# Optimization experiments

Hardware: AMD Instinct MI355X
Metric: run time of the kernel (lower is better)

Reference implementation:

```python
import jax, jax.numpy as jnp
import numpy as np

N = 100000   # nodes
E = 1200000  # edges
D = 64       # feature dim (in_channels == out_channels)


def gcn_layer(x, W, src, dst):
    # GCNConv(normalize=False, bias=False, aggr='add'):
    # linear transform then scatter-add of source messages into targets.
    h = x @ W                                            # [N, D]
    msg = h[src]                                         # [E, D] gather
    return jax.ops.segment_sum(msg, dst, num_segments=x.shape[0])  # [N, D]


def setup_inputs() -> dict:
    key = jax.random.key(0)
    ks = jax.random.split(key, 5)
    x = jax.random.normal(ks[0], (N, D), dtype=jnp.float32)
    edge_index = jax.random.randint(ks[1], (2, E), 0, N, dtype=jnp.int64)
    scale = 1.0 / np.sqrt(D).astype(np.float32)
    W0 = jax.random.normal(ks[2], (D, D), dtype=jnp.float32) * scale
    W1 = jax.random.normal(ks[3], (D, D), dtype=jnp.float32) * scale
    W2 = jax.random.normal(ks[4], (D, D), dtype=jnp.float32) * scale
    return {"x": x, "edge_index": edge_index, "W0": W0, "W1": W1, "W2": W2}


def reference(x, edge_index, W0, W1, W2):
    src = edge_index[0]  # messages flow source -> target (PyG default)
    dst = edge_index[1]
    # num_hop = 3 stacked convs; dropout p=0 and use_bn=False are no-ops.
    for W in (W0, W1, W2):
        x = gcn_layer(x, W, src, dst)
    return x
```

## Files before the change

kernel.cpp:

```cpp
#include <hip/hip_runtime.h>


#define GCN_D 64
#define SEGSHIFT 8
#define SEGROWS 256
#define MAXSEG 512
#define A_EPB 4096

typedef unsigned short ushort;

__device__ __forceinline__ float bf2f(ushort u) {
    union { unsigned u; float f; } c; c.u = ((unsigned)u) << 16; return c.f;
}
__device__ __forceinline__ ushort f2bf(float f) {
    union { float f; unsigned u; } c; c.f = f;
    const unsigned r = 0x7FFFu + ((c.u >> 16) & 1u);
    return (ushort)((c.u + r) >> 16);
}

__global__ __launch_bounds__(256) void k_wchain(const float* __restrict__ W0,
                                                const float* __restrict__ W1,
                                                const float* __restrict__ W2,
                                                float* __restrict__ Wc) {
    __shared__ float A[4096], B[4096], T[4096];
    const int t = threadIdx.x;
    for (int i = t; i < 1024; i += 256) {
        ((float4*)A)[i] = ((const float4*)W0)[i];
        ((float4*)B)[i] = ((const float4*)W1)[i];
    }
    __syncthreads();
#pragma unroll
    for (int g = 0; g < 4; ++g) {
        const int idx = t + 256 * g;
        const int r = idx >> 4, c4 = idx & 15;
        float4 acc = make_float4(0.f, 0.f, 0.f, 0.f);
#pragma unroll
        for (int k = 0; k < 64; ++k) {
            const float a = A[r * 64 + k];
            const float4 b = ((float4*)B)[k * 16 + c4];
            acc.x = fmaf(a, b.x, acc.x); acc.y = fmaf(a, b.y, acc.y);
            acc.z = fmaf(a, b.z, acc.z); acc.w = fmaf(a, b.w, acc.w);
        }
        ((float4*)T)[idx] = acc;
    }
    __syncthreads();
    for (int i = t; i < 1024; i += 256) ((float4*)B)[i] = ((const float4*)W2)[i];
    __syncthreads();
#pragma unroll
    for (int g = 0; g < 4; ++g) {
        const int idx = t + 256 * g;
        const int r = idx >> 4, c4 = idx & 15;
        float4 acc = make_float4(0.f, 0.f, 0.f, 0.f);
#pragma unroll
        for (int k = 0; k < 64; ++k) {
            const float a = T[r * 64 + k];
            const float4 b = ((float4*)B)[k * 16 + c4];
            acc.x = fmaf(a, b.x, acc.x); acc.y = fmaf(a, b.y, acc.y);
            acc.z = fmaf(a, b.z, acc.z); acc.w = fmaf(a, b.w, acc.w);
        }
        ((float4*)Wc)[idx] = acc;
    }
}

__global__ __launch_bounds__(256) void k_tobf(const float* __restrict__ X,
                                              ushort* __restrict__ B,
                                              int* __restrict__ ghist, long long n4) {
    if (blockIdx.x == 0) {
        for (int i = threadIdx.x; i < MAXSEG; i += 256) ghist[i] = 0;
    }
    const long long stride = (long long)gridDim.x * 256;
    for (long long i = blockIdx.x * 256ll + threadIdx.x; i < n4; i += stride) {
        const float4 v = ((const float4*)X)[i];
        ushort4 u;
        u.x = f2bf(v.x); u.y = f2bf(v.y); u.z = f2bf(v.z); u.w = f2bf(v.w);
        ((ushort4*)B)[i] = u;
    }
}

__global__ __launch_bounds__(256) void k_a0(const int* __restrict__ ei,
                                            int* __restrict__ ghist, int E) {
    __shared__ int h[MAXSEG];
    const int t = threadIdx.x;
    for (int i = t; i < MAXSEG; i += 256) h[i] = 0;
    __syncthreads();
    for (int e = blockIdx.x * 256 + t; e < E; e += gridDim.x * 256)
        atomicAdd(&h[ei[E + e] >> SEGSHIFT], 1);
    __syncthreads();
    for (int i = t; i < MAXSEG; i += 256) {
        const int c = h[i];
        if (c) atomicAdd(&ghist[i], c);
    }
}

__global__ __launch_bounds__(MAXSEG) void k_ascan(const int* __restrict__ ghist,
                                                  int* __restrict__ gOff,
                                                  int* __restrict__ gcur,
                                                  int* __restrict__ rp, int N, int E) {
    __shared__ int sd[MAXSEG];
    const int t = threadIdx.x;
    const int v = ghist[t];
    sd[t] = v; __syncthreads();
    for (int off = 1; off < MAXSEG; off <<= 1) {
        const int y = (t >= off) ? sd[t - off] : 0;
        __syncthreads();
        sd[t] += y;
        __syncthreads();
    }
    const int excl = sd[t] - v;
    gOff[t] = excl; gcur[t] = excl;
    if (t == MAXSEG - 1) gOff[MAXSEG] = sd[t];
    if (t == 0) rp[N] = E;
}

__global__ __launch_bounds__(512) void k_apart(const int* __restrict__ ei,
                                               int* __restrict__ gcur,
                                               unsigned* __restrict__ ebuf, int E) {
    __shared__ int hist[MAXSEG], lofs[MAXSEG], cur[MAXSEG], gbase[MAXSEG];
    __shared__ unsigned stg[A_EPB];
    const int t = threadIdx.x;
    const int base = blockIdx.x * A_EPB;
    const int cnt = min(A_EPB, E - base);

    hist[t] = 0;
    __syncthreads();

    unsigned my[8]; int mb[8];
#pragma unroll
    for (int j = 0; j < 8; ++j) {
        const int i = t + j * 512;
        if (i < cnt) {
            const int e = base + i;
            const unsigned s = (unsigned)ei[e];
            const unsigned d = (unsigned)ei[E + e];
            my[j] = (s << 8) | (d & (SEGROWS - 1));
            mb[j] = (int)(d >> SEGSHIFT);
            atomicAdd(&hist[mb[j]], 1);
        } else mb[j] = -1;
    }
    __syncthreads();

    {
        const int v = hist[t];
        lofs[t] = v; __syncthreads();
        for (int off = 1; off < MAXSEG; off <<= 1) {
            const int y = (t >= off) ? lofs[t - off] : 0;
            __syncthreads();
            lofs[t] += y;
            __syncthreads();
        }
        const int excl = lofs[t] - v;
        __syncthreads();
        lofs[t] = excl; cur[t] = excl;
    }
    __syncthreads();

#pragma unroll
    for (int j = 0; j < 8; ++j) {
        if (mb[j] >= 0) {
            const int p = atomicAdd(&cur[mb[j]], 1);
            stg[p] = my[j];
        }
    }
    __syncthreads();

    {
        const int c = hist[t];
        gbase[t] = c ? atomicAdd(&gcur[t], c) : 0;
    }
    __syncthreads();

    for (int i = t; i < cnt; i += 512) {
        int lo = 0, hi = MAXSEG - 1;
        while (lo < hi) {
            const int mid = (lo + hi + 1) >> 1;
            if (lofs[mid] <= i) lo = mid; else hi = mid - 1;
        }
        ebuf[(size_t)gbase[lo] + (unsigned)(i - lofs[lo])] = stg[i];
    }
}

__global__ __launch_bounds__(SEGROWS) void k_bplace(const unsigned* __restrict__ ebuf,
                                                    const int* __restrict__ gOff,
                                                    int* __restrict__ rp,
                                                    int* __restrict__ cs, int N) {
    __shared__ int h[SEGROWS], ofs[SEGROWS];
    const int s = blockIdx.x;
    const int t = threadIdx.x;
    const int e0 = gOff[s];
    const int e1 = gOff[s + 1];

    h[t] = 0; __syncthreads();
    for (int e = e0 + t; e < e1; e += SEGROWS)
        atomicAdd(&h[ebuf[e] & (SEGROWS - 1)], 1);
    __syncthreads();

    const int v = h[t];
    ofs[t] = v; __syncthreads();
    for (int off = 1; off < SEGROWS; off <<= 1) {
        const int y = (t >= off) ? ofs[t - off] : 0;
        __syncthreads();
        ofs[t] += y;
        __syncthreads();
    }
    const int excl = ofs[t] - v;
    const int r = s * SEGROWS + t;
    if (r < N) rp[r] = e0 + excl;
    __syncthreads();
    ofs[t] = excl;
    __syncthreads();

    for (int e = e0 + t; e < e1; e += SEGROWS) {
        const unsigned pr = ebuf[e];
        const int lr = (int)(pr & (SEGROWS - 1));
        const int p = atomicAdd(&ofs[lr], 1);
        cs[e0 + p] = (int)(pr >> 8);
    }
}

__global__ __launch_bounds__(256) void k_aggc(const ushort* __restrict__ B,
                                              const int* __restrict__ rp,
                                              const int* __restrict__ cs,
                                              ushort* __restrict__ out, int N) {
    const int t = threadIdx.x;
    const int gw = (blockIdx.x * 256 + t) >> 6;
    const int lane = t & 63;
    const int f4 = lane & 15;
    const int r = gw * 4 + (lane >> 4);
    if (r >= N) return;

    const int e0 = rp[r];
    const int e1 = rp[r + 1];
    const ushort4* Bv = (const ushort4*)B;

    float4 acc = make_float4(0.f, 0.f, 0.f, 0.f);
    int e = e0;
    for (; e + 7 < e1; e += 8) {
        ushort4 u[8];
#pragma unroll
        for (int j = 0; j < 8; ++j) u[j] = Bv[(size_t)cs[e + j] * 16 + f4];
#pragma unroll
        for (int j = 0; j < 8; ++j) {
            acc.x += bf2f(u[j].x); acc.y += bf2f(u[j].y);
            acc.z += bf2f(u[j].z); acc.w += bf2f(u[j].w);
        }
    }
    for (; e + 3 < e1; e += 4) {
        ushort4 u[4];
#pragma unroll
        for (int j = 0; j < 4; ++j) u[j] = Bv[(size_t)cs[e + j] * 16 + f4];
#pragma unroll
        for (int j = 0; j < 4; ++j) {
            acc.x += bf2f(u[j].x); acc.y += bf2f(u[j].y);
            acc.z += bf2f(u[j].z); acc.w += bf2f(u[j].w);
        }
    }
    for (; e < e1; ++e) {
        const ushort4 u = Bv[(size_t)cs[e] * 16 + f4];
        acc.x += bf2f(u.x); acc.y += bf2f(u.y);
        acc.z += bf2f(u.z); acc.w += bf2f(u.w);
    }
    ushort4 o;
    o.x = f2bf(acc.x); o.y = f2bf(acc.y); o.z = f2bf(acc.z); o.w = f2bf(acc.w);
    ((ushort4*)out)[(size_t)r * 16 + f4] = o;
}

__global__ __launch_bounds__(256) void k_aggf(const ushort* __restrict__ B,
                                              const int* __restrict__ rp,
                                              const int* __restrict__ cs,
                                              const float* __restrict__ Wc,
                                              float* __restrict__ out, int N) {
    __shared__ float Wl[64 * 64];
    __shared__ float Xl[16][65];
    const int t = threadIdx.x;
    for (int i = t; i < 1024; i += 256) ((float4*)Wl)[i] = ((const float4*)Wc)[i];

    const int lr = t >> 4;
    const int f4 = t & 15;
    const int r = blockIdx.x * 16 + lr;

    float4 acc = make_float4(0.f, 0.f, 0.f, 0.f);
    if (r < N) {
        const int e0 = rp[r];
        const int e1 = rp[r + 1];
        const ushort4* Bv = (const ushort4*)B;
        int e = e0;
        for (; e + 7 < e1; e += 8) {
            ushort4 u[8];
#pragma unroll
            for (int j = 0; j < 8; ++j) u[j] = Bv[(size_t)cs[e + j] * 16 + f4];
#pragma unroll
            for (int j = 0; j < 8; ++j) {
                acc.x += bf2f(u[j].x); acc.y += bf2f(u[j].y);
                acc.z += bf2f(u[j].z); acc.w += bf2f(u[j].w);
            }
        }
        for (; e + 3 < e1; e += 4) {
            ushort4 u[4];
#pragma unroll
            for (int j = 0; j < 4; ++j) u[j] = Bv[(size_t)cs[e + j] * 16 + f4];
#pragma unroll
            for (int j = 0; j < 4; ++j) {
                acc.x += bf2f(u[j].x); acc.y += bf2f(u[j].y);
                acc.z += bf2f(u[j].z); acc.w += bf2f(u[j].w);
            }
        }
        for (; e < e1; ++e) {
            const ushort4 u = Bv[(size_t)cs[e] * 16 + f4];
            acc.x += bf2f(u.x); acc.y += bf2f(u.y);
            acc.z += bf2f(u.z); acc.w += bf2f(u.w);
        }
    }
    Xl[lr][f4 * 4 + 0] = bf2f(f2bf(acc.x));
    Xl[lr][f4 * 4 + 1] = bf2f(f2bf(acc.y));
    Xl[lr][f4 * 4 + 2] = bf2f(f2bf(acc.z));
    Xl[lr][f4 * 4 + 3] = bf2f(f2bf(acc.w));
    __syncthreads();

    float4 g = make_float4(0.f, 0.f, 0.f, 0.f);
#pragma unroll
    for (int k = 0; k < 64; ++k) {
        const float xv = Xl[lr][k];
        const float4 w4 = ((const float4*)Wl)[k * 16 + f4];
        g.x = fmaf(xv, w4.x, g.x); g.y = fmaf(xv, w4.y, g.y);
        g.z = fmaf(xv, w4.z, g.z); g.w = fmaf(xv, w4.w, g.w);
    }
    if (r < N) ((float4*)out)[(size_t)r * 16 + f4] = g;
}

__global__ __launch_bounds__(256) void gcn_gemm64(const float* __restrict__ X,
                                                  const float* __restrict__ W,
                                                  float* __restrict__ H,
                                                  int nrows) {
    __shared__ float Wl[64 * 64];
    __shared__ float Xl[16][65];
    const int tid = threadIdx.x;
    for (int i = tid; i < 1024; i += 256) ((float4*)Wl)[i] = ((const float4*)W)[i];
    const int rowBase = blockIdx.x * 16;
    const int lr = tid >> 4;
    const int lc = tid & 15;
    const int grow = rowBase + lr;
    if (grow < nrows) {
        float4 xv = ((const float4*)X)[(long long)grow * 16 + lc];
        Xl[lr][lc * 4 + 0] = xv.x; Xl[lr][lc * 4 + 1] = xv.y;
        Xl[lr][lc * 4 + 2] = xv.z; Xl[lr][lc * 4 + 3] = xv.w;
    }
    __syncthreads();
    float4 acc = make_float4(0.f, 0.f, 0.f, 0.f);
#pragma unroll
    for (int k = 0; k < 64; ++k) {
        const float xv = Xl[lr][k];
        const float4 w4 = ((float4*)Wl)[k * 16 + lc];
        acc.x = fmaf(xv, w4.x, acc.x); acc.y = fmaf(xv, w4.y, acc.y);
        acc.z = fmaf(xv, w4.z, acc.z); acc.w = fmaf(xv, w4.w, acc.w);
    }
    if (grow < nrows) ((float4*)H)[(long long)grow * 16 + lc] = acc;
}

__global__ __launch_bounds__(256) void gcn_scatter(const float* __restrict__ H,
                                                   const int* __restrict__ ei,
                                                   float* __restrict__ out,
                                                   int nedges) {
    const long long t = (long long)blockIdx.x * 256 + threadIdx.x;
    const int e = (int)(t >> 4);
    if (e >= nedges) return;
    const int lc = (int)(t & 15);
    const int s = ei[e];
    const int d = ei[nedges + e];
    const float4 v = ((const float4*)H)[(long long)s * 16 + lc];
    float* o = out + (long long)d * GCN_D + lc * 4;
    atomicAdd(o + 0, v.x);
    atomicAdd(o + 1, v.y);
    atomicAdd(o + 2, v.z);
    atomicAdd(o + 3, v.w);
}

extern "C" void kernel_launch(void* const* d_in, const int* in_sizes, int n_in,
                              void* d_out, int out_size, void* d_ws, size_t ws_size,
                              hipStream_t stream) {
    const float* x  = (const float*)d_in[0];
    const int*   ei = (const int*)d_in[1];
    const float* W0 = (const float*)d_in[2];
    const float* W1 = (const float*)d_in[3];
    const float* W2 = (const float*)d_in[4];
    float* out = (float*)d_out;

    const int N_ = in_sizes[0] / GCN_D;
    const int E_ = in_sizes[1] / 2;
    const int NSEG = (N_ + SEGROWS - 1) >> SEGSHIFT;

    uintptr_t base = (uintptr_t)d_ws;
    ushort* B0 = (ushort*)base;
    const size_t bfBytes  = (size_t)N_ * GCN_D * 2;
    const size_t regBytes = bfBytes > (size_t)E_ * 4 ? bfBytes : (size_t)E_ * 4;
    ushort*   B1   = (ushort*)(base + bfBytes);
    unsigned* ebuf = (unsigned*)B1;
    int* rp    = (int*)(base + bfBytes + regBytes);
    int* gOff  = rp + (N_ + 2);
    int* ghist = gOff + (MAXSEG + 1);
    int* gcur  = ghist + MAXSEG;
    float* Wc  = (float*)(gcur + MAXSEG);
    int* cs    = (int*)(Wc + 4096);
    const size_t needed = ((uintptr_t)(cs + E_) - base);

    const int gemmBlocks = (N_ + 15) / 16;

    if (NSEG <= MAXSEG && N_ < (1 << 24) && ws_size >= needed) {
        k_wchain<<<1, 256, 0, stream>>>(W0, W1, W2, Wc);
        k_tobf<<<1024, 256, 0, stream>>>(x, B0, ghist, (long long)N_ * 16);
        k_a0<<<512, 256, 0, stream>>>(ei, ghist, E_);
        k_ascan<<<1, MAXSEG, 0, stream>>>(ghist, gOff, gcur, rp, N_, E_);
        k_apart<<<(E_ + A_EPB - 1) / A_EPB, 512, 0, stream>>>(ei, gcur, ebuf, E_);
        k_bplace<<<NSEG, SEGROWS, 0, stream>>>(ebuf, gOff, rp, cs, N_);

        const int aggBlocks = (N_ + 15) / 16;
        k_aggc<<<aggBlocks, 256, 0, stream>>>(B0, rp, cs, B1, N_);
        k_aggc<<<aggBlocks, 256, 0, stream>>>(B1, rp, cs, B0, N_);
        k_aggf<<<aggBlocks, 256, 0, stream>>>(B0, rp, cs, Wc, out, N_);
    } else {
        float* h = (float*)d_ws;
        const int scatBlocks = (int)(((long long)E_ * 16 + 255) / 256);
        const float* curAct = x;
        for (int l = 0; l < 3; ++l) {
            const float* Wl = (l == 0) ? W0 : (l == 1) ? W1 : W2;
            gcn_gemm64<<<gemmBlocks, 256, 0, stream>>>(curAct, Wl, h, N_);
            hipMemsetAsync(out, 0, (size_t)N_ * GCN_D * sizeof(float), stream);
            gcn_scatter<<<scatBlocks, 256, 0, stream>>>(h, ei, out, E_);
            curAct = out;
        }
    }
}
```

Baseline: 177.1 us.

## Apply combined weight before aggregation and drop binary search in partition

The product of the three weight matrices is now applied to x up front in a GEMM that writes bf16, replacing the plain bf16 conversion. This leaves the last aggregation as a pure gather-sum with no shared-memory GEMM or block barrier. It relies on the layers being linear, and it changes where bf16 rounding happens relative to the reference. Separately, the partition kernel stores each edge's bucket id in shared memory, replacing a per-element binary search over bucket offsets, and the histogram zeroing moves into the weight-chain kernel.

Measured after the change: 172.4 us. -2.7%, faster.

```diff
diff --git a/kernel.cpp b/kernel.cpp
--- a/kernel.cpp
+++ b/kernel.cpp
@@ -21,9 +21,11 @@
 __global__ __launch_bounds__(256) void k_wchain(const float* __restrict__ W0,
                                                 const float* __restrict__ W1,
                                                 const float* __restrict__ W2,
-                                                float* __restrict__ Wc) {
+                                                float* __restrict__ Wc,
+                                                int* __restrict__ ghist) {
     __shared__ float A[4096], B[4096], T[4096];
     const int t = threadIdx.x;
+    for (int i = t; i < MAXSEG; i += 256) ghist[i] = 0;
     for (int i = t; i < 1024; i += 256) {
         ((float4*)A)[i] = ((const float4*)W0)[i];
         ((float4*)B)[i] = ((const float4*)W1)[i];
@@ -62,18 +64,38 @@
     }
 }
 
-__global__ __launch_bounds__(256) void k_tobf(const float* __restrict__ X,
-                                              ushort* __restrict__ B,
-                                              int* __restrict__ ghist, long long n4) {
-    if (blockIdx.x == 0) {
-        for (int i = threadIdx.x; i < MAXSEG; i += 256) ghist[i] = 0;
-    }
-    const long long stride = (long long)gridDim.x * 256;
-    for (long long i = blockIdx.x * 256ll + threadIdx.x; i < n4; i += stride) {
-        const float4 v = ((const float4*)X)[i];
-        ushort4 u;
-        u.x = f2bf(v.x); u.y = f2bf(v.y); u.z = f2bf(v.z); u.w = f2bf(v.w);
-        ((ushort4*)B)[i] = u;
+__global__ __launch_bounds__(256) void k_gemmcvt(const float* __restrict__ X,
+                                                 const float* __restrict__ Wc,
+                                                 ushort* __restrict__ B,
+                                                 int nrows) {
+    __shared__ float Wl[64 * 64];
+    __shared__ float Xl[16][65];
+    const int tid = threadIdx.x;
+    for (int i = tid; i < 1024; i += 256) ((float4*)Wl)[i] = ((const float4*)Wc)[i];
+
+    const int lr = tid >> 4;
+    const int lc = tid & 15;
+    const int grow = blockIdx.x * 16 + lr;
+
+    if (grow < nrows) {
+        const float4 xv = ((const float4*)X)[(size_t)grow * 16 + lc];
+        Xl[lr][lc * 4 + 0] = xv.x; Xl[lr][lc * 4 + 1] = xv.y;
+        Xl[lr][lc * 4 + 2] = xv.z; Xl[lr][lc * 4 + 3] = xv.w;
+    }
+    __syncthreads();
+
+    float4 acc = make_float4(0.f, 0.f, 0.f, 0.f);
+#pragma unroll
+    for (int k = 0; k < 64; ++k) {
+        const float xv = Xl[lr][k];
+        const float4 w4 = ((const float4*)Wl)[k * 16 + lc];
+        acc.x = fmaf(xv, w4.x, acc.x); acc.y = fmaf(xv, w4.y, acc.y);
+        acc.z = fmaf(xv, w4.z, acc.z); acc.w = fmaf(xv, w4.w, acc.w);
+    }
+    if (grow < nrows) {
+        ushort4 o;
+        o.x = f2bf(acc.x); o.y = f2bf(acc.y); o.z = f2bf(acc.z); o.w = f2bf(acc.w);
+        ((ushort4*)B)[(size_t)grow * 16 + lc] = o;
     }
 }
 
@@ -117,6 +139,7 @@
                                                unsigned* __restrict__ ebuf, int E) {
     __shared__ int hist[MAXSEG], lofs[MAXSEG], cur[MAXSEG], gbase[MAXSEG];
     __shared__ unsigned stg[A_EPB];
+    __shared__ ushort stg2[A_EPB];
     const int t = threadIdx.x;
     const int base = blockIdx.x * A_EPB;
     const int cnt = min(A_EPB, E - base);
@@ -159,6 +182,7 @@
         if (mb[j] >= 0) {
             const int p = atomicAdd(&cur[mb[j]], 1);
             stg[p] = my[j];
+            stg2[p] = (ushort)mb[j];
         }
     }
     __syncthreads();
@@ -170,12 +194,8 @@
     __syncthreads();
 
     for (int i = t; i < cnt; i += 512) {
-        int lo = 0, hi = MAXSEG - 1;
-        while (lo < hi) {
-            const int mid = (lo + hi + 1) >> 1;
-            if (lofs[mid] <= i) lo = mid; else hi = mid - 1;
-        }
-        ebuf[(size_t)gbase[lo] + (unsigned)(i - lofs[lo])] = stg[i];
+        const int b = (int)stg2[i];
+        ebuf[(size_t)gbase[b] + (unsigned)(i - lofs[b])] = stg[i];
     }
 }
 
@@ -264,67 +284,49 @@
     ((ushort4*)out)[(size_t)r * 16 + f4] = o;
 }
 
-__global__ __launch_bounds__(256) void k_aggf(const ushort* __restrict__ B,
+__global__ __launch_bounds__(256) void k_aggw(const ushort* __restrict__ B,
                                               const int* __restrict__ rp,
                                               const int* __restrict__ cs,
-                                              const float* __restrict__ Wc,
                                               float* __restrict__ out, int N) {
-    __shared__ float Wl[64 * 64];
-    __shared__ float Xl[16][65];
-    const int t = threadIdx.x;
-    for (int i = t; i < 1024; i += 256) ((float4*)Wl)[i] = ((const float4*)Wc)[i];
-
-    const int lr = t >> 4;
-    const int f4 = t & 15;
-    const int r = blockIdx.x * 16 + lr;
+    const int t = threadIdx.x;
+    const int gw = (blockIdx.x * 256 + t) >> 6;
+    const int lane = t & 63;
+    const int f4 = lane & 15;
+    const int r = gw * 4 + (lane >> 4);
+    if (r >= N) return;
+
+    const int e0 = rp[r];
+    const int e1 = rp[r + 1];
+    const ushort4* Bv = (const ushort4*)B;
 
     float4 acc = make_float4(0.f, 0.f, 0.f, 0.f);
-    if (r < N) {
-        const int e0 = rp[r];
-        const int e1 = rp[r + 1];
-        const ushort4* Bv = (const ushort4*)B;
-        int e = e0;
-        for (; e + 7 < e1; e += 8) {
-            ushort4 u[8];
-#pragma unroll
-            for (int j = 0; j < 8; ++j) u[j] = Bv[(size_t)cs[e + j] * 16 + f4];
-#pragma unroll
-            for (int j = 0; j < 8; ++j) {
-                acc.x += bf2f(u[j].x); acc.y += bf2f(u[j].y);
-                acc.z += bf2f(u[j].z); acc.w += bf2f(u[j].w);
-            }
-        }
-        for (; e + 3 < e1; e += 4) {
-            ushort4 u[4];
-#pragma unroll
-            for (int j = 0; j < 4; ++j) u[j] = Bv[(size_t)cs[e + j] * 16 + f4];
-#pragma unroll
-            for (int j = 0; j < 4; ++j) {
-                acc.x += bf2f(u[j].x); acc.y += bf2f(u[j].y);
-                acc.z += bf2f(u[j].z); acc.w += bf2f(u[j].w);
-            }
-        }
-        for (; e < e1; ++e) {
-            const ushort4 u = Bv[(size_t)cs[e] * 16 + f4];
-            acc.x += bf2f(u.x); acc.y += bf2f(u.y);
-            acc.z += bf2f(u.z); acc.w += bf2f(u.w);
-        }
-    }
-    Xl[lr][f4 * 4 + 0] = bf2f(f2bf(acc.x));
-    Xl[lr][f4 * 4 + 1] = bf2f(f2bf(acc.y));
-    Xl[lr][f4 * 4 + 2] = bf2f(f2bf(acc.z));
-    Xl[lr][f4 * 4 + 3] = bf2f(f2bf(acc.w));
-    __syncthreads();
-
-    float4 g = make_float4(0.f, 0.f, 0.f, 0.f);
-#pragma unroll
-    for (int k = 0; k < 64; ++k) {
-        const float xv = Xl[lr][k];
-        const float4 w4 = ((const float4*)Wl)[k * 16 + f4];
-        g.x = fmaf(xv, w4.x, g.x); g.y = fmaf(xv, w4.y, g.y);
-        g.z = fmaf(xv, w4.z, g.z); g.w = fmaf(xv, w4.w, g.w);
-    }
-    if (r < N) ((float4*)out)[(size_t)r * 16 + f4] = g;
+    int e = e0;
+    for (; e + 7 < e1; e += 8) {
+        ushort4 u[8];
+#pragma unroll
+        for (int j = 0; j < 8; ++j) u[j] = Bv[(size_t)cs[e + j] * 16 + f4];
+#pragma unroll
+        for (int j = 0; j < 8; ++j) {
+            acc.x += bf2f(u[j].x); acc.y += bf2f(u[j].y);
+            acc.z += bf2f(u[j].z); acc.w += bf2f(u[j].w);
+        }
+    }
+    for (; e + 3 < e1; e += 4) {
+        ushort4 u[4];
+#pragma unroll
+        for (int j = 0; j < 4; ++j) u[j] = Bv[(size_t)cs[e + j] * 16 + f4];
+#pragma unroll
+        for (int j = 0; j < 4; ++j) {
+            acc.x += bf2f(u[j].x); acc.y += bf2f(u[j].y);
+            acc.z += bf2f(u[j].z); acc.w += bf2f(u[j].w);
+        }
+    }
+    for (; e < e1; ++e) {
+        const ushort4 u = Bv[(size_t)cs[e] * 16 + f4];
+        acc.x += bf2f(u.x); acc.y += bf2f(u.y);
+        acc.z += bf2f(u.z); acc.w += bf2f(u.w);
+    }
+    ((float4*)out)[(size_t)r * 16 + f4] = acc;
 }
 
 __global__ __launch_bounds__(256) void gcn_gemm64(const float* __restrict__ X,
@@ -405,8 +407,8 @@
     const int gemmBlocks = (N_ + 15) / 16;
 
     if (NSEG <= MAXSEG && N_ < (1 << 24) && ws_size >= needed) {
-        k_wchain<<<1, 256, 0, stream>>>(W0, W1, W2, Wc);
-        k_tobf<<<1024, 256, 0, stream>>>(x, B0, ghist, (long long)N_ * 16);
+        k_wchain<<<1, 256, 0, stream>>>(W0, W1, W2, Wc, ghist);
+        k_gemmcvt<<<gemmBlocks, 256, 0, stream>>>(x, Wc, B0, N_);
         k_a0<<<512, 256, 0, stream>>>(ei, ghist, E_);
         k_ascan<<<1, MAXSEG, 0, stream>>>(ghist, gOff, gcur, rp, N_, E_);
         k_apart<<<(E_ + A_EPB - 1) / A_EPB, 512, 0, stream>>>(ei, gcur, ebuf, E_);
@@ -415,7 +417,7 @@
         const int aggBlocks = (N_ + 15) / 16;
         k_aggc<<<aggBlocks, 256, 0, stream>>>(B0, rp, cs, B1, N_);
         k_aggc<<<aggBlocks, 256, 0, stream>>>(B1, rp, cs, B0, N_);
-        k_aggf<<<aggBlocks, 256, 0, stream>>>(B0, rp, cs, Wc, out, N_);
+        k_aggw<<<aggBlocks, 256, 0, stream>>>(B0, rp, cs, out, N_);
     } else {
         float* h = (float*)d_ws;
         const int scatBlocks = (int)(((long long)E_ * 16 + 255) / 256);
```
